# Performance work log

Measured on AMD Instinct MI355X. Metric: run time of the kernel, lower is better.

Reference implementation:

```python
import jax, jax.numpy as jnp
import numpy as np

N_NODES = 50000
N_EDGES = 800000
IN_DIM, HID_DIM, OUT_DIM = 1024, 256, 512


def setup_inputs() -> dict:
    key = jax.random.key(0)
    ks = jax.random.split(key, 8)
    x = jax.random.normal(ks[0], (N_NODES, IN_DIM), dtype=jnp.float32)
    edge_index = jax.random.randint(ks[1], (2, N_EDGES), 0, N_NODES, dtype=jnp.int64)
    # Glorot-ish scaled weights; PyG SAGEConv: out = lin_l(mean_aggr) + lin_r(x), bias in lin_l
    w1_l = jax.random.normal(ks[2], (HID_DIM, IN_DIM), dtype=jnp.float32) / np.sqrt(IN_DIM)
    w1_r = jax.random.normal(ks[3], (HID_DIM, IN_DIM), dtype=jnp.float32) / np.sqrt(IN_DIM)
    b1 = jnp.zeros((HID_DIM,), dtype=jnp.float32)
    w2_l = jax.random.normal(ks[4], (OUT_DIM, HID_DIM), dtype=jnp.float32) / np.sqrt(HID_DIM)
    w2_r = jax.random.normal(ks[5], (OUT_DIM, HID_DIM), dtype=jnp.float32) / np.sqrt(HID_DIM)
    b2 = jnp.zeros((OUT_DIM,), dtype=jnp.float32)
    return {"x": x, "edge_index": edge_index, "w1_l": w1_l, "w1_r": w1_r, "b1": b1,
            "w2_l": w2_l, "w2_r": w2_r, "b2": b2}


def _sage_conv(x, edge_index, w_l, w_r, b):
    """PyG SAGEConv with mean aggregation: lin_l(mean_{j in N(i)} x_j) + lin_r(x_i)."""
    src, dst = edge_index[0], edge_index[1]
    n = x.shape[0]
    # gather source features and scatter-mean into destinations (the memory-bound part)
    agg = jax.ops.segment_sum(x[src], dst, num_segments=n)          # [N, d_in]
    cnt = jax.ops.segment_sum(jnp.ones_like(src, dtype=x.dtype), dst, num_segments=n)
    mean = agg / jnp.maximum(cnt, 1.0)[:, None]                     # empty neighborhoods -> 0
    return mean @ w_l.T + x @ w_r.T + b


def reference(x, edge_index, w1_l, w1_r, b1, w2_l, w2_r, b2):
    # layer 1 + relu (dropout is identity in eval mode)
    h = jax.nn.relu(_sage_conv(x, edge_index, w1_l, w1_r, b1))
    # final layer, no activation
    return _sage_conv(h, edge_index, w2_l, w2_r, b2)
```

## Files before the change

### kernel.cpp

```cpp
#include <hip/hip_runtime.h>


#define IN_DIM  1024
#define HID_DIM 256
#define OUT_N   512

typedef __attribute__((ext_vector_type(8))) short bf16x8;
typedef __attribute__((ext_vector_type(4))) float f32x4;

static __device__ __forceinline__ unsigned short f2bf(float f) {
  unsigned int u = __float_as_uint(f);
  u += 0x7fffu + ((u >> 16) & 1u);
  return (unsigned short)(u >> 16);
}
static __device__ __forceinline__ float bf2f(unsigned short b) {
  return __uint_as_float(((unsigned int)b) << 16);
}

static __device__ __forceinline__ int load_idx(const void* ei, long long pos, int is64) {
  if (is64) return (int)((const long long*)ei)[pos];
  return ((const int*)ei)[pos];
}

__global__ void k_pre(const unsigned int* __restrict__ eiu, const void* __restrict__ ei,
                      int* __restrict__ flag,
                      const float* __restrict__ w1l, const float* __restrict__ w1r,
                      unsigned short* __restrict__ W1c,
                      const float* __restrict__ w2l, const float* __restrict__ w2r,
                      unsigned short* __restrict__ W2c,
                      const float* __restrict__ x, unsigned short* __restrict__ xbf,
                      int n4, int nxb, int nE, int* __restrict__ deg) {
  int b = blockIdx.x;
  if (b == 0) {
    if (threadIdx.x < 64) {
      unsigned int v = eiu[2 * threadIdx.x + 1];
      unsigned long long m = __ballot(v == 0u);
      if (threadIdx.x == 0) *flag = (m == ~0ull) ? 1 : 0;
    }
    return;
  }
  if (b < 513) {
    int i = (b - 1) * 256 + threadIdx.x;
    int base = i * 4;
    int n = base / IN_DIM, k = base % IN_DIM;
    const float* s = (n < HID_DIM) ? &w1l[(size_t)n * IN_DIM + k]
                                   : &w1r[(size_t)(n - HID_DIM) * IN_DIM + k];
    float4 v = *(const float4*)s;
    ushort4 o = { f2bf(v.x), f2bf(v.y), f2bf(v.z), f2bf(v.w) };
    *(ushort4*)&W1c[base] = o;
    return;
  }
  if (b < 769) {
    int i = (b - 513) * 256 + threadIdx.x;
    int base = i * 4;
    int n = base >> 9, k = base & 511;
    const float* s = (k < HID_DIM) ? &w2l[(size_t)n * HID_DIM + k]
                                   : &w2r[(size_t)n * HID_DIM + (k - HID_DIM)];
    float4 v = *(const float4*)s;
    ushort4 o = { f2bf(v.x), f2bf(v.y), f2bf(v.z), f2bf(v.w) };
    *(ushort4*)&W2c[base] = o;
    return;
  }
  if (b < 769 + nxb) {
    int i = (b - 769) * 256 + threadIdx.x;
    if (i >= n4) return;
    float4 v = ((const float4*)x)[i];
    ushort4 o = { f2bf(v.x), f2bf(v.y), f2bf(v.z), f2bf(v.w) };
    ((ushort4*)xbf)[i] = o;
    return;
  }
  __shared__ int s_is64;
  if (threadIdx.x < 64) {
    unsigned int v = eiu[2 * threadIdx.x + 1];
    unsigned long long m = __ballot(v == 0u);
    if (threadIdx.x == 0) s_is64 = (m == ~0ull) ? 1 : 0;
  }
  __syncthreads();
  int e = (b - 769 - nxb) * 256 + threadIdx.x;
  if (e < nE) {
    int d = load_idx(ei, (long long)nE + e, s_is64);
    atomicAdd(&deg[d], 1);
  }
}

__global__ void k_bsum(const int* __restrict__ deg, int* __restrict__ bsum) {
  int t = threadIdx.x;
  int4 d4 = ((const int4*)(deg + (size_t)blockIdx.x * 1024))[t];
  int v = d4.x + d4.y + d4.z + d4.w;
#pragma unroll
  for (int d = 1; d < 64; d <<= 1) v += __shfl_xor(v, d);
  __shared__ int ws[4];
  if ((t & 63) == 0) ws[t >> 6] = v;
  __syncthreads();
  if (t == 0) bsum[blockIdx.x] = ws[0] + ws[1] + ws[2] + ws[3];
}

__global__ __launch_bounds__(1024) void k_bscan(int* __restrict__ bsum, int nb) {
  __shared__ int s[1024];
  int t = threadIdx.x;
  s[t] = (t < nb) ? bsum[t] : 0;
  __syncthreads();
  for (int d = 1; d < 1024; d <<= 1) {
    int v = (t >= d) ? s[t - d] : 0;
    __syncthreads();
    s[t] += v;
    __syncthreads();
  }
  if (t < nb) bsum[t] = s[t];
}

__global__ __launch_bounds__(256) void k_offsets(const int* __restrict__ deg,
                                                 const int* __restrict__ bsumInc,
                                                 int* __restrict__ off,
                                                 int* __restrict__ cursor) {
  const int t = threadIdx.x;
  const int l = t & 63, w = t >> 6;
  const size_t base = (size_t)blockIdx.x * 1024;
  int4 d4 = ((const int4*)(deg + base))[t];
  int tsum = d4.x + d4.y + d4.z + d4.w;
  int incl = tsum;
#pragma unroll
  for (int d = 1; d < 64; d <<= 1) {
    int u = __shfl_up(incl, d);
    if (l >= d) incl += u;
  }
  __shared__ int wt[4];
  if (l == 63) wt[w] = incl;
  __syncthreads();
  int wpre = 0;
  for (int i = 0; i < w; ++i) wpre += wt[i];
  int bpre = (blockIdx.x == 0) ? 0 : bsumInc[blockIdx.x - 1];
  int excl = bpre + wpre + incl - tsum;
  int4 o;
  o.x = excl;
  o.y = excl + d4.x;
  o.z = o.y + d4.y;
  o.w = o.z + d4.z;
  ((int4*)(off + base))[t] = o;
  ((int4*)(cursor + base))[t] = o;
}

__global__ void k_fill(const void* ei, int nE, const int* flag,
                       int* cursor, int* __restrict__ csr) {
  int e = blockIdx.x * 256 + threadIdx.x;
  if (e >= nE) return;
  int is64 = *flag;
  int s = load_idx(ei, e, is64);
  int d = load_idx(ei, (long long)nE + e, is64);
  int p = atomicAdd(&cursor[d], 1);
  csr[p] = s;
}

static __device__ __forceinline__ void load_lds16(const void* g, void* lds) {
  __builtin_amdgcn_global_load_lds(
      (const __attribute__((address_space(1))) unsigned int*)g,
      (__attribute__((address_space(3))) unsigned int*)lds, 16, 0, 0);
}

static __device__ __forceinline__ int xcd_swz(int orig, int nwg) {
  const int q = nwg >> 3, r = nwg & 7;
  const int xcd = orig & 7, rk = orig >> 3;
  return (xcd < r) ? xcd * (q + 1) + rk : r * (q + 1) + (xcd - r) * q + rk;
}

__global__ __launch_bounds__(256) void k_gemm1(const unsigned short* __restrict__ A,
                                               const unsigned short* __restrict__ B,
                                               unsigned short* __restrict__ Cl,
                                               unsigned short* __restrict__ Cr,
                                               const float* __restrict__ b1) {
  __shared__ unsigned short As[128 * 32];
  __shared__ unsigned short Bs[128 * 32];
  const int tid = threadIdx.x;
  const int w = tid >> 6, l = tid & 63;
  const int wm = w >> 1, wn = w & 1;
  const int quad = l >> 4, lane16 = l & 15;
  const int nwg = gridDim.x * gridDim.y;
  const int wg = xcd_swz(blockIdx.y * gridDim.x + blockIdx.x, nwg);
  const int m0 = (wg / gridDim.x) * 128;
  const int n0 = (wg % gridDim.x) * 128;

  f32x4 acc[4][4] = {};
  for (int k0 = 0; k0 < IN_DIM; k0 += 32) {
#pragma unroll
    for (int c = 0; c < 2; ++c) {
      const int flat = ((w * 2 + c) << 10);
      const int fb = flat + l * 16;
      const int row = fb >> 6;
      const int cb = fb & 63;
      load_lds16(A + (size_t)(m0 + row) * IN_DIM + (k0 + (cb >> 1)), (char*)As + flat);
      load_lds16(B + (size_t)(n0 + row) * IN_DIM + (k0 + (cb >> 1)), (char*)Bs + flat);
    }
    __syncthreads();
    bf16x8 af[4], bfr[4];
#pragma unroll
    for (int i = 0; i < 4; ++i)
      af[i] = *(const bf16x8*)&As[(wm * 64 + i * 16 + lane16) * 32 + quad * 8];
#pragma unroll
    for (int j = 0; j < 4; ++j)
      bfr[j] = *(const bf16x8*)&Bs[(wn * 64 + j * 16 + lane16) * 32 + quad * 8];
#pragma unroll
    for (int i = 0; i < 4; ++i)
#pragma unroll
      for (int j = 0; j < 4; ++j)
        acc[i][j] = __builtin_amdgcn_mfma_f32_16x16x32_bf16(af[i], bfr[j], acc[i][j], 0, 0, 0);
    __syncthreads();
  }

  const bool right = (n0 >= 256);
  unsigned short* Cb = right ? Cr : Cl;
  const int nc0 = n0 - (right ? 256 : 0);
#pragma unroll
  for (int i = 0; i < 4; ++i) {
    const int rbase = m0 + wm * 64 + i * 16 + quad * 4;
#pragma unroll
    for (int j = 0; j < 4; ++j) {
      const int col = nc0 + wn * 64 + j * 16 + lane16;
      const float bv = right ? b1[col] : 0.0f;
#pragma unroll
      for (int r = 0; r < 4; ++r)
        Cb[(size_t)(rbase + r) * HID_DIM + col] = f2bf(acc[i][j][r] + bv);
    }
  }
}

__global__ __launch_bounds__(256) void k_gemm2(const unsigned short* __restrict__ Am,
                                               const unsigned short* __restrict__ Ah,
                                               const unsigned short* __restrict__ B,
                                               float* __restrict__ out,
                                               const float* __restrict__ b2, int Mstore) {
  __shared__ unsigned short As[128 * 32];
  __shared__ unsigned short Bs[128 * 32];
  const int tid = threadIdx.x;
  const int w = tid >> 6, l = tid & 63;
  const int wm = w >> 1, wn = w & 1;
  const int quad = l >> 4, lane16 = l & 15;
  const int nwg = gridDim.x * gridDim.y;
  const int wg = xcd_swz(blockIdx.y * gridDim.x + blockIdx.x, nwg);
  const int m0 = (wg / gridDim.x) * 128;
  const int n0 = (wg % gridDim.x) * 128;

  f32x4 acc[4][4] = {};
  for (int k0 = 0; k0 < 2 * HID_DIM; k0 += 32) {
    const unsigned short* Abase = (k0 < HID_DIM) ? Am + k0 : Ah + (k0 - HID_DIM);
#pragma unroll
    for (int c = 0; c < 2; ++c) {
      const int flat = ((w * 2 + c) << 10);
      const int fb = flat + l * 16;
      const int row = fb >> 6;
      const int cb = fb & 63;
      load_lds16(Abase + (size_t)(m0 + row) * HID_DIM + (cb >> 1), (char*)As + flat);
      load_lds16(B + (size_t)(n0 + row) * (2 * HID_DIM) + (k0 + (cb >> 1)), (char*)Bs + flat);
    }
    __syncthreads();
    bf16x8 af[4], bfr[4];
#pragma unroll
    for (int i = 0; i < 4; ++i)
      af[i] = *(const bf16x8*)&As[(wm * 64 + i * 16 + lane16) * 32 + quad * 8];
#pragma unroll
    for (int j = 0; j < 4; ++j)
      bfr[j] = *(const bf16x8*)&Bs[(wn * 64 + j * 16 + lane16) * 32 + quad * 8];
#pragma unroll
    for (int i = 0; i < 4; ++i)
#pragma unroll
      for (int j = 0; j < 4; ++j)
        acc[i][j] = __builtin_amdgcn_mfma_f32_16x16x32_bf16(af[i], bfr[j], acc[i][j], 0, 0, 0);
    __syncthreads();
  }

#pragma unroll
  for (int i = 0; i < 4; ++i) {
    const int rbase = m0 + wm * 64 + i * 16 + quad * 4;
#pragma unroll
    for (int j = 0; j < 4; ++j) {
      const int col = n0 + wn * 64 + j * 16 + lane16;
      const float bv = b2[col];
#pragma unroll
      for (int r = 0; r < 4; ++r) {
        const int rowi = rbase + r;
        if (rowi < Mstore) out[(size_t)rowi * OUT_N + col] = acc[i][j][r] + bv;
      }
    }
  }
}

template <int NB>
static __device__ __forceinline__ void gatherN(const unsigned short* __restrict__ src,
                                               const int* __restrict__ csr, int ib,
                                               size_t colb, float* a) {
  bf16x8 v[NB];
#pragma unroll
  for (int u = 0; u < NB; ++u) {
    int r = csr[ib + 2 * u];
    v[u] = *(const bf16x8*)&src[(size_t)r * HID_DIM + colb];
  }
#pragma unroll
  for (int u = 0; u < NB; ++u)
#pragma unroll
    for (int c = 0; c < 8; ++c) a[c] += bf2f((unsigned short)v[u][c]);
}

static __device__ __forceinline__ void agg_sum(const unsigned short* __restrict__ src,
                                               const int* __restrict__ csr,
                                               int s, int e, int half, size_t colb,
                                               float* a) {
  const int cnt = e - s;
  const int P = cnt >> 1;
  const int ib0 = s + half;
  int k = 0;
  for (; k + 8 <= P; k += 8) gatherN<8>(src, csr, ib0 + 2 * k, colb, a);
  if (k + 4 <= P) { gatherN<4>(src, csr, ib0 + 2 * k, colb, a); k += 4; }
  if (k + 2 <= P) { gatherN<2>(src, csr, ib0 + 2 * k, colb, a); k += 2; }
  if (k < P)      { gatherN<1>(src, csr, ib0 + 2 * k, colb, a); }
  if ((cnt & 1) && half == 0) {
    bf16x8 v = *(const bf16x8*)&src[(size_t)csr[e - 1] * HID_DIM + colb];
#pragma unroll
    for (int c = 0; c < 8; ++c) a[c] += bf2f((unsigned short)v[c]);
  }
#pragma unroll
  for (int c = 0; c < 8; ++c) a[c] += __shfl_xor(a[c], 32);
}

__global__ void k_agg1(const unsigned short* __restrict__ Cl,
                       const unsigned short* __restrict__ Cr,
                       const int* __restrict__ off, const int* __restrict__ csr,
                       unsigned short* __restrict__ h, int nNodes) {
  int node = blockIdx.x * 4 + (threadIdx.x >> 6);
  if (node >= nNodes) return;
  const int l = threadIdx.x & 63;
  const int half = l >> 5, li = l & 31;
  const size_t colb = (size_t)li * 8;
  int s = off[node], e = off[node + 1];
  float a[8] = {};
  agg_sum(Cl, csr, s, e, half, colb, a);
  if (half == 0) {
    float inv = 1.0f / fmaxf((float)(e - s), 1.0f);
    bf16x8 xr = *(const bf16x8*)&Cr[(size_t)node * HID_DIM + colb];
    bf16x8 o;
#pragma unroll
    for (int c = 0; c < 8; ++c)
      o[c] = (short)f2bf(fmaxf(a[c] * inv + bf2f((unsigned short)xr[c]), 0.0f));
    *(bf16x8*)&h[(size_t)node * HID_DIM + colb] = o;
  }
}

__global__ void k_agg2(const unsigned short* __restrict__ hsrc,
                       const int* __restrict__ off, const int* __restrict__ csr,
                       unsigned short* __restrict__ mean2, int nNodes) {
  int node = blockIdx.x * 4 + (threadIdx.x >> 6);
  if (node >= nNodes) return;
  const int l = threadIdx.x & 63;
  const int half = l >> 5, li = l & 31;
  const size_t colb = (size_t)li * 8;
  int s = off[node], e = off[node + 1];
  float a[8] = {};
  agg_sum(hsrc, csr, s, e, half, colb, a);
  if (half == 0) {
    float inv = 1.0f / fmaxf((float)(e - s), 1.0f);
    bf16x8 o;
#pragma unroll
    for (int c = 0; c < 8; ++c) o[c] = (short)f2bf(a[c] * inv);
    *(bf16x8*)&mean2[(size_t)node * HID_DIM + colb] = o;
  }
}

extern "C" void kernel_launch(void* const* d_in, const int* in_sizes, int n_in,
                              void* d_out, int out_size, void* d_ws, size_t ws_size,
                              hipStream_t stream) {
  const float* x   = (const float*)d_in[0];
  const void*  ei  = d_in[1];
  const float* w1l = (const float*)d_in[2];
  const float* w1r = (const float*)d_in[3];
  const float* b1  = (const float*)d_in[4];
  const float* w2l = (const float*)d_in[5];
  const float* w2r = (const float*)d_in[6];
  const float* b2  = (const float*)d_in[7];
  float* out = (float*)d_out;

  const int nN   = in_sizes[0] / IN_DIM;
  const int nE   = in_sizes[1] / 2;
  const int Mpad = (nN + 127) & ~127;
  const int padN = (nN + 1023) & ~1023;
  const int nb   = padN >> 10;

  char* ws = (char*)d_ws;
  size_t o = 0;
  auto alloc = [&](size_t bytes) {
    char* p = ws + o;
    o += (bytes + 255) & ~(size_t)255;
    return p;
  };
  unsigned short* xbf   = (unsigned short*)alloc((size_t)Mpad * IN_DIM * 2);
  unsigned short* W1c   = (unsigned short*)alloc((size_t)2 * HID_DIM * IN_DIM * 2);
  unsigned short* W2c   = (unsigned short*)alloc((size_t)OUT_N * 2 * HID_DIM * 2);
  unsigned short* Cl    = (unsigned short*)alloc((size_t)Mpad * HID_DIM * 2);
  unsigned short* Cr    = (unsigned short*)alloc((size_t)Mpad * HID_DIM * 2);
  unsigned short* hbuf  = (unsigned short*)alloc((size_t)Mpad * HID_DIM * 2);
  unsigned short* mean2 = (unsigned short*)alloc((size_t)Mpad * HID_DIM * 2);
  int* deg    = (int*)alloc((size_t)padN * 4);
  int* offs   = (int*)alloc((size_t)padN * 4);
  int* cursor = (int*)alloc((size_t)padN * 4);
  int* bsum   = (int*)alloc((size_t)1024 * 4);
  int* csr    = (int*)alloc((size_t)nE * 4);
  int* flag   = (int*)alloc(256);

  hipMemsetAsync(deg, 0, (size_t)padN * 4, stream);

  const int n4  = nN * IN_DIM / 4;
  const int nxb = (n4 + 255) / 256;
  const int nEb = (nE + 255) / 256;
  k_pre<<<769 + nxb + nEb, 256, 0, stream>>>((const unsigned int*)ei, ei, flag,
                                             w1l, w1r, W1c, w2l, w2r, W2c,
                                             x, xbf, n4, nxb, nE, deg);
  k_bsum<<<nb, 256, 0, stream>>>(deg, bsum);
  k_bscan<<<1, 1024, 0, stream>>>(bsum, nb);
  k_offsets<<<nb, 256, 0, stream>>>(deg, bsum, offs, cursor);
  k_fill<<<(nE + 255) / 256, 256, 0, stream>>>(ei, nE, flag, cursor, csr);

  dim3 g1(512 / 128, Mpad / 128);
  k_gemm1<<<g1, 256, 0, stream>>>(xbf, W1c, Cl, Cr, b1);
  k_agg1<<<(nN + 3) / 4, 256, 0, stream>>>(Cl, Cr, offs, csr, hbuf, nN);
  k_agg2<<<(nN + 3) / 4, 256, 0, stream>>>(hbuf, offs, csr, mean2, nN);
  k_gemm2<<<g1, 256, 0, stream>>>(mean2, hbuf, W2c, out, b2, nN);
}
```

Measured before the change: 667.7 us.

## Fuse x bf16 conversion into GEMM1, merge scan kernels, overlap CSR fill

Drops the separate pass that converted x to bf16. GEMM1 now loads fp32 x directly, converts it in registers and stores it to LDS, which saves a full write and re-read of a 100MB-class intermediate. The three-kernel degree prefix scan becomes a single one-block scan kernel. The CSR fill runs as extra blocks appended to the GEMM1 grid so it overlaps the GEMM. In exchange, the A loads in the GEMM lose async direct-to-LDS transfer and become synchronous, and the single-block scan serializes roughly 50K entries.

Result: no change. 654.9 us (-1.9%).

```diff
diff --git a/kernel.cpp b/kernel.cpp
--- a/kernel.cpp
+++ b/kernel.cpp
@@ -28,8 +28,7 @@
                       unsigned short* __restrict__ W1c,
                       const float* __restrict__ w2l, const float* __restrict__ w2r,
                       unsigned short* __restrict__ W2c,
-                      const float* __restrict__ x, unsigned short* __restrict__ xbf,
-                      int n4, int nxb, int nE, int* __restrict__ deg) {
+                      int nE, int* __restrict__ deg) {
   int b = blockIdx.x;
   if (b == 0) {
     if (threadIdx.x < 64) {
@@ -61,14 +60,6 @@
     *(ushort4*)&W2c[base] = o;
     return;
   }
-  if (b < 769 + nxb) {
-    int i = (b - 769) * 256 + threadIdx.x;
-    if (i >= n4) return;
-    float4 v = ((const float4*)x)[i];
-    ushort4 o = { f2bf(v.x), f2bf(v.y), f2bf(v.z), f2bf(v.w) };
-    ((ushort4*)xbf)[i] = o;
-    return;
-  }
   __shared__ int s_is64;
   if (threadIdx.x < 64) {
     unsigned int v = eiu[2 * threadIdx.x + 1];
@@ -76,79 +67,51 @@
     if (threadIdx.x == 0) s_is64 = (m == ~0ull) ? 1 : 0;
   }
   __syncthreads();
-  int e = (b - 769 - nxb) * 256 + threadIdx.x;
+  int e = (b - 769) * 256 + threadIdx.x;
   if (e < nE) {
     int d = load_idx(ei, (long long)nE + e, s_is64);
     atomicAdd(&deg[d], 1);
   }
 }
 
-__global__ void k_bsum(const int* __restrict__ deg, int* __restrict__ bsum) {
-  int t = threadIdx.x;
-  int4 d4 = ((const int4*)(deg + (size_t)blockIdx.x * 1024))[t];
-  int v = d4.x + d4.y + d4.z + d4.w;
-#pragma unroll
-  for (int d = 1; d < 64; d <<= 1) v += __shfl_xor(v, d);
-  __shared__ int ws[4];
-  if ((t & 63) == 0) ws[t >> 6] = v;
-  __syncthreads();
-  if (t == 0) bsum[blockIdx.x] = ws[0] + ws[1] + ws[2] + ws[3];
-}
-
-__global__ __launch_bounds__(1024) void k_bscan(int* __restrict__ bsum, int nb) {
+__global__ __launch_bounds__(1024) void k_scan1(const int* __restrict__ deg,
+                                                int* __restrict__ off,
+                                                int* __restrict__ cursor, int n4q) {
+  const int t = threadIdx.x;
+  const int CH = (n4q + 1023) >> 10;
+  const int i0 = t * CH;
+  int tsum = 0;
+  for (int i = 0; i < CH; ++i) {
+    int idx = i0 + i;
+    if (idx < n4q) {
+      int4 d = ((const int4*)deg)[idx];
+      tsum += d.x + d.y + d.z + d.w;
+    }
+  }
   __shared__ int s[1024];
-  int t = threadIdx.x;
-  s[t] = (t < nb) ? bsum[t] : 0;
+  s[t] = tsum;
   __syncthreads();
   for (int d = 1; d < 1024; d <<= 1) {
-    int v = (t >= d) ? s[t - d] : 0;
-    __syncthreads();
-    s[t] += v;
-    __syncthreads();
-  }
-  if (t < nb) bsum[t] = s[t];
-}
-
-__global__ __launch_bounds__(256) void k_offsets(const int* __restrict__ deg,
-                                                 const int* __restrict__ bsumInc,
-                                                 int* __restrict__ off,
-                                                 int* __restrict__ cursor) {
-  const int t = threadIdx.x;
-  const int l = t & 63, w = t >> 6;
-  const size_t base = (size_t)blockIdx.x * 1024;
-  int4 d4 = ((const int4*)(deg + base))[t];
-  int tsum = d4.x + d4.y + d4.z + d4.w;
-  int incl = tsum;
-#pragma unroll
-  for (int d = 1; d < 64; d <<= 1) {
-    int u = __shfl_up(incl, d);
-    if (l >= d) incl += u;
-  }
-  __shared__ int wt[4];
-  if (l == 63) wt[w] = incl;
-  __syncthreads();
-  int wpre = 0;
-  for (int i = 0; i < w; ++i) wpre += wt[i];
-  int bpre = (blockIdx.x == 0) ? 0 : bsumInc[blockIdx.x - 1];
-  int excl = bpre + wpre + incl - tsum;
-  int4 o;
-  o.x = excl;
-  o.y = excl + d4.x;
-  o.z = o.y + d4.y;
-  o.w = o.z + d4.z;
-  ((int4*)(off + base))[t] = o;
-  ((int4*)(cursor + base))[t] = o;
-}
-
-__global__ void k_fill(const void* ei, int nE, const int* flag,
-                       int* cursor, int* __restrict__ csr) {
-  int e = blockIdx.x * 256 + threadIdx.x;
-  if (e >= nE) return;
-  int is64 = *flag;
-  int s = load_idx(ei, e, is64);
-  int d = load_idx(ei, (long long)nE + e, is64);
-  int p = atomicAdd(&cursor[d], 1);
-  csr[p] = s;
+    int u = (t >= d) ? s[t - d] : 0;
+    __syncthreads();
+    s[t] += u;
+    __syncthreads();
+  }
+  int run = (t == 0) ? 0 : s[t - 1];
+  for (int i = 0; i < CH; ++i) {
+    int idx = i0 + i;
+    if (idx < n4q) {
+      int4 d = ((const int4*)deg)[idx];
+      int4 o;
+      o.x = run;
+      o.y = run + d.x;
+      o.z = o.y + d.y;
+      o.w = o.z + d.z;
+      run = o.w + d.w;
+      ((int4*)off)[idx] = o;
+      ((int4*)cursor)[idx] = o;
+    }
+  }
 }
 
 static __device__ __forceinline__ void load_lds16(const void* g, void* lds) {
@@ -163,31 +126,61 @@
   return (xcd < r) ? xcd * (q + 1) + rk : r * (q + 1) + (xcd - r) * q + rk;
 }
 
-__global__ __launch_bounds__(256) void k_gemm1(const unsigned short* __restrict__ A,
-                                               const unsigned short* __restrict__ B,
-                                               unsigned short* __restrict__ Cl,
-                                               unsigned short* __restrict__ Cr,
-                                               const float* __restrict__ b1) {
+__global__ __launch_bounds__(256) void k_g1f(const float* __restrict__ A,
+                                             const unsigned short* __restrict__ B,
+                                             unsigned short* __restrict__ Cl,
+                                             unsigned short* __restrict__ Cr,
+                                             const float* __restrict__ b1,
+                                             int nNm1, int ngemm,
+                                             const void* __restrict__ ei, int nE,
+                                             const int* __restrict__ flag,
+                                             int* __restrict__ cursor,
+                                             int* __restrict__ csr) {
+  if ((int)blockIdx.x >= ngemm) {
+    int e = ((int)blockIdx.x - ngemm) * 256 + threadIdx.x;
+    if (e < nE) {
+      int is64 = *flag;
+      int s = load_idx(ei, e, is64);
+      int d = load_idx(ei, (long long)nE + e, is64);
+      int p = atomicAdd(&cursor[d], 1);
+      csr[p] = s;
+    }
+    return;
+  }
   __shared__ unsigned short As[128 * 32];
   __shared__ unsigned short Bs[128 * 32];
   const int tid = threadIdx.x;
   const int w = tid >> 6, l = tid & 63;
   const int wm = w >> 1, wn = w & 1;
   const int quad = l >> 4, lane16 = l & 15;
-  const int nwg = gridDim.x * gridDim.y;
-  const int wg = xcd_swz(blockIdx.y * gridDim.x + blockIdx.x, nwg);
-  const int m0 = (wg / gridDim.x) * 128;
-  const int n0 = (wg % gridDim.x) * 128;
+  const int wg = xcd_swz(blockIdx.x, ngemm);
+  const int m0 = (wg >> 2) * 128;
+  const int n0 = (wg & 3) * 128;
+
+  const float* ap[4];
+#pragma unroll
+  for (int it = 0; it < 4; ++it) {
+    const int eidx = it * 1024 + tid * 4;
+    int ar = m0 + (eidx >> 5);
+    if (ar > nNm1) ar = nNm1;
+    ap[it] = A + (size_t)ar * IN_DIM + (eidx & 31);
+  }
 
   f32x4 acc[4][4] = {};
   for (int k0 = 0; k0 < IN_DIM; k0 += 32) {
+#pragma unroll
+    for (int it = 0; it < 4; ++it) {
+      const int eidx = it * 1024 + tid * 4;
+      float4 v = *(const float4*)(ap[it] + k0);
+      ushort4 o = { f2bf(v.x), f2bf(v.y), f2bf(v.z), f2bf(v.w) };
+      *(ushort4*)&As[eidx] = o;
+    }
 #pragma unroll
     for (int c = 0; c < 2; ++c) {
       const int flat = ((w * 2 + c) << 10);
       const int fb = flat + l * 16;
       const int row = fb >> 6;
       const int cb = fb & 63;
-      load_lds16(A + (size_t)(m0 + row) * IN_DIM + (k0 + (cb >> 1)), (char*)As + flat);
       load_lds16(B + (size_t)(n0 + row) * IN_DIM + (k0 + (cb >> 1)), (char*)Bs + flat);
     }
     __syncthreads();
@@ -380,7 +373,6 @@
   const int nE   = in_sizes[1] / 2;
   const int Mpad = (nN + 127) & ~127;
   const int padN = (nN + 1023) & ~1023;
-  const int nb   = padN >> 10;
 
   char* ws = (char*)d_ws;
   size_t o = 0;
@@ -389,7 +381,6 @@
     o += (bytes + 255) & ~(size_t)255;
     return p;
   };
-  unsigned short* xbf   = (unsigned short*)alloc((size_t)Mpad * IN_DIM * 2);
   unsigned short* W1c   = (unsigned short*)alloc((size_t)2 * HID_DIM * IN_DIM * 2);
   unsigned short* W2c   = (unsigned short*)alloc((size_t)OUT_N * 2 * HID_DIM * 2);
   unsigned short* Cl    = (unsigned short*)alloc((size_t)Mpad * HID_DIM * 2);
@@ -399,26 +390,21 @@
   int* deg    = (int*)alloc((size_t)padN * 4);
   int* offs   = (int*)alloc((size_t)padN * 4);
   int* cursor = (int*)alloc((size_t)padN * 4);
-  int* bsum   = (int*)alloc((size_t)1024 * 4);
   int* csr    = (int*)alloc((size_t)nE * 4);
   int* flag   = (int*)alloc(256);
 
   hipMemsetAsync(deg, 0, (size_t)padN * 4, stream);
 
-  const int n4  = nN * IN_DIM / 4;
-  const int nxb = (n4 + 255) / 256;
-  const int nEb = (nE + 255) / 256;
-  k_pre<<<769 + nxb + nEb, 256, 0, stream>>>((const unsigned int*)ei, ei, flag,
-                                             w1l, w1r, W1c, w2l, w2r, W2c,
-                                             x, xbf, n4, nxb, nE, deg);
-  k_bsum<<<nb, 256, 0, stream>>>(deg, bsum);
-  k_bscan<<<1, 1024, 0, stream>>>(bsum, nb);
-  k_offsets<<<nb, 256, 0, stream>>>(deg, bsum, offs, cursor);
-  k_fill<<<(nE + 255) / 256, 256, 0, stream>>>(ei, nE, flag, cursor, csr);
-
-  dim3 g1(512 / 128, Mpad / 128);
-  k_gemm1<<<g1, 256, 0, stream>>>(xbf, W1c, Cl, Cr, b1);
+  const int nEb   = (nE + 255) / 256;
+  const int ngemm = 4 * (Mpad / 128);
+
+  k_pre<<<769 + nEb, 256, 0, stream>>>((const unsigned int*)ei, ei, flag,
+                                       w1l, w1r, W1c, w2l, w2r, W2c, nE, deg);
+  k_scan1<<<1, 1024, 0, stream>>>(deg, offs, cursor, padN / 4);
+  k_g1f<<<ngemm + nEb, 256, 0, stream>>>(x, W1c, Cl, Cr, b1, nN - 1, ngemm,
+                                         ei, nE, flag, cursor, csr);
   k_agg1<<<(nN + 3) / 4, 256, 0, stream>>>(Cl, Cr, offs, csr, hbuf, nN);
   k_agg2<<<(nN + 3) / 4, 256, 0, stream>>>(hbuf, offs, csr, mean2, nN);
-  k_gemm2<<<g1, 256, 0, stream>>>(mean2, hbuf, W2c, out, b2, nN);
-}
+  dim3 g2(512 / 128, Mpad / 128);
+  k_gemm2<<<g2, 256, 0, stream>>>(mean2, hbuf, W2c, out, b2, nN);
+}
```

## Double-buffer GEMM LDS tiles and fuse CSR fill into GEMM1 launch

Applied to the files above, without the earlier changes.

Both GEMM kernels now use two LDS buffers, so the tile for the next K step is loaded while MFMAs run on the current one, with one barrier per iteration instead of two. The CSR fill kernel is merged into the first GEMM launch as extra blocks, so the atomic edge scatter runs alongside the GEMM instead of as a separate launch. This doubles LDS per block, which may lower occupancy, and the fill blocks compete with GEMM blocks for CUs.

Result: no change. 675.2 us (+1.1%).

```diff
diff --git a/kernel.cpp b/kernel.cpp
--- a/kernel.cpp
+++ b/kernel.cpp
@@ -140,17 +140,6 @@
   ((int4*)(cursor + base))[t] = o;
 }
 
-__global__ void k_fill(const void* ei, int nE, const int* flag,
-                       int* cursor, int* __restrict__ csr) {
-  int e = blockIdx.x * 256 + threadIdx.x;
-  if (e >= nE) return;
-  int is64 = *flag;
-  int s = load_idx(ei, e, is64);
-  int d = load_idx(ei, (long long)nE + e, is64);
-  int p = atomicAdd(&cursor[d], 1);
-  csr[p] = s;
-}
-
 static __device__ __forceinline__ void load_lds16(const void* g, void* lds) {
   __builtin_amdgcn_global_load_lds(
       (const __attribute__((address_space(1))) unsigned int*)g,
@@ -163,13 +152,98 @@
   return (xcd < r) ? xcd * (q + 1) + rk : r * (q + 1) + (xcd - r) * q + rk;
 }
 
-__global__ __launch_bounds__(256) void k_gemm1(const unsigned short* __restrict__ A,
+__global__ __launch_bounds__(256) void k_g1f(const unsigned short* __restrict__ A,
+                                             const unsigned short* __restrict__ B,
+                                             unsigned short* __restrict__ Cl,
+                                             unsigned short* __restrict__ Cr,
+                                             const float* __restrict__ b1,
+                                             int ngemm,
+                                             const void* __restrict__ ei, int nE,
+                                             const int* __restrict__ flag,
+                                             int* __restrict__ cursor,
+                                             int* __restrict__ csr) {
+  if ((int)blockIdx.x >= ngemm) {
+    int e = ((int)blockIdx.x - ngemm) * 256 + threadIdx.x;
+    if (e < nE) {
+      int is64 = *flag;
+      int s = load_idx(ei, e, is64);
+      int d = load_idx(ei, (long long)nE + e, is64);
+      int p = atomicAdd(&cursor[d], 1);
+      csr[p] = s;
+    }
+    return;
+  }
+  __shared__ unsigned short As[2][128 * 32];
+  __shared__ unsigned short Bs[2][128 * 32];
+  const int tid = threadIdx.x;
+  const int w = tid >> 6, l = tid & 63;
+  const int wm = w >> 1, wn = w & 1;
+  const int quad = l >> 4, lane16 = l & 15;
+  const int wg = xcd_swz(blockIdx.x, ngemm);
+  const int m0 = (wg >> 2) * 128;
+  const int n0 = (wg & 3) * 128;
+
+  const int flat0 = ((w * 2 + 0) << 10), flat1 = ((w * 2 + 1) << 10);
+  const int row0 = (flat0 + l * 16) >> 6, cb0 = (flat0 + l * 16) & 63;
+  const int row1 = (flat1 + l * 16) >> 6, cb1 = (flat1 + l * 16) & 63;
+  const unsigned short* Ar0 = A + (size_t)(m0 + row0) * IN_DIM + (cb0 >> 1);
+  const unsigned short* Ar1 = A + (size_t)(m0 + row1) * IN_DIM + (cb1 >> 1);
+  const unsigned short* Br0 = B + (size_t)(n0 + row0) * IN_DIM + (cb0 >> 1);
+  const unsigned short* Br1 = B + (size_t)(n0 + row1) * IN_DIM + (cb1 >> 1);
+
+  auto STAGE = [&](int k0, int buf) {
+    load_lds16(Ar0 + k0, (char*)As[buf] + flat0);
+    load_lds16(Br0 + k0, (char*)Bs[buf] + flat0);
+    load_lds16(Ar1 + k0, (char*)As[buf] + flat1);
+    load_lds16(Br1 + k0, (char*)Bs[buf] + flat1);
+  };
+
+  f32x4 acc[4][4] = {};
+  STAGE(0, 0);
+  __syncthreads();
+  int cur = 0;
+  for (int k0 = 0; k0 < IN_DIM; k0 += 32) {
+    if (k0 + 32 < IN_DIM) STAGE(k0 + 32, cur ^ 1);
+    bf16x8 af[4], bfr[4];
+#pragma unroll
+    for (int i = 0; i < 4; ++i)
+      af[i] = *(const bf16x8*)&As[cur][(wm * 64 + i * 16 + lane16) * 32 + quad * 8];
+#pragma unroll
+    for (int j = 0; j < 4; ++j)
+      bfr[j] = *(const bf16x8*)&Bs[cur][(wn * 64 + j * 16 + lane16) * 32 + quad * 8];
+#pragma unroll
+    for (int i = 0; i < 4; ++i)
+#pragma unroll
+      for (int j = 0; j < 4; ++j)
+        acc[i][j] = __builtin_amdgcn_mfma_f32_16x16x32_bf16(af[i], bfr[j], acc[i][j], 0, 0, 0);
+    __syncthreads();
+    cur ^= 1;
+  }
+
+  const bool right = (n0 >= 256);
+  unsigned short* Cb = right ? Cr : Cl;
+  const int nc0 = n0 - (right ? 256 : 0);
+#pragma unroll
+  for (int i = 0; i < 4; ++i) {
+    const int rbase = m0 + wm * 64 + i * 16 + quad * 4;
+#pragma unroll
+    for (int j = 0; j < 4; ++j) {
+      const int col = nc0 + wn * 64 + j * 16 + lane16;
+      const float bv = right ? b1[col] : 0.0f;
+#pragma unroll
+      for (int r = 0; r < 4; ++r)
+        Cb[(size_t)(rbase + r) * HID_DIM + col] = f2bf(acc[i][j][r] + bv);
+    }
+  }
+}
+
+__global__ __launch_bounds__(256) void k_gemm2(const unsigned short* __restrict__ Am,
+                                               const unsigned short* __restrict__ Ah,
                                                const unsigned short* __restrict__ B,
-                                               unsigned short* __restrict__ Cl,
-                                               unsigned short* __restrict__ Cr,
-                                               const float* __restrict__ b1) {
-  __shared__ unsigned short As[128 * 32];
-  __shared__ unsigned short Bs[128 * 32];
+                                               float* __restrict__ out,
+                                               const float* __restrict__ b2, int Mstore) {
+  __shared__ unsigned short As[2][128 * 32];
+  __shared__ unsigned short Bs[2][128 * 32];
   const int tid = threadIdx.x;
   const int w = tid >> 6, l = tid & 63;
   const int wm = w >> 1, wn = w & 1;
@@ -179,92 +253,38 @@
   const int m0 = (wg / gridDim.x) * 128;
   const int n0 = (wg % gridDim.x) * 128;
 
+  const int flat0 = ((w * 2 + 0) << 10), flat1 = ((w * 2 + 1) << 10);
+  const int row0 = (flat0 + l * 16) >> 6, cb0 = (flat0 + l * 16) & 63;
+  const int row1 = (flat1 + l * 16) >> 6, cb1 = (flat1 + l * 16) & 63;
+
+  auto STAGE = [&](int kk, int buf) {
+    const unsigned short* Abase = (kk < HID_DIM) ? Am + kk : Ah + (kk - HID_DIM);
+    load_lds16(Abase + (size_t)(m0 + row0) * HID_DIM + (cb0 >> 1), (char*)As[buf] + flat0);
+    load_lds16(B + (size_t)(n0 + row0) * (2 * HID_DIM) + (kk + (cb0 >> 1)), (char*)Bs[buf] + flat0);
+    load_lds16(Abase + (size_t)(m0 + row1) * HID_DIM + (cb1 >> 1), (char*)As[buf] + flat1);
+    load_lds16(B + (size_t)(n0 + row1) * (2 * HID_DIM) + (kk + (cb1 >> 1)), (char*)Bs[buf] + flat1);
+  };
+
   f32x4 acc[4][4] = {};
-  for (int k0 = 0; k0 < IN_DIM; k0 += 32) {
-#pragma unroll
-    for (int c = 0; c < 2; ++c) {
-      const int flat = ((w * 2 + c) << 10);
-      const int fb = flat + l * 16;
-      const int row = fb >> 6;
-      const int cb = fb & 63;
-      load_lds16(A + (size_t)(m0 + row) * IN_DIM + (k0 + (cb >> 1)), (char*)As + flat);
-      load_lds16(B + (size_t)(n0 + row) * IN_DIM + (k0 + (cb >> 1)), (char*)Bs + flat);
-    }
-    __syncthreads();
+  STAGE(0, 0);
+  __syncthreads();
+  int cur = 0;
+  for (int k0 = 0; k0 < 2 * HID_DIM; k0 += 32) {
+    if (k0 + 32 < 2 * HID_DIM) STAGE(k0 + 32, cur ^ 1);
     bf16x8 af[4], bfr[4];
 #pragma unroll
     for (int i = 0; i < 4; ++i)
-      af[i] = *(const bf16x8*)&As[(wm * 64 + i * 16 + lane16) * 32 + quad * 8];
+      af[i] = *(const bf16x8*)&As[cur][(wm * 64 + i * 16 + lane16) * 32 + quad * 8];
 #pragma unroll
     for (int j = 0; j < 4; ++j)
-      bfr[j] = *(const bf16x8*)&Bs[(wn * 64 + j * 16 + lane16) * 32 + quad * 8];
+      bfr[j] = *(const bf16x8*)&Bs[cur][(wn * 64 + j * 16 + lane16) * 32 + quad * 8];
 #pragma unroll
     for (int i = 0; i < 4; ++i)
 #pragma unroll
       for (int j = 0; j < 4; ++j)
         acc[i][j] = __builtin_amdgcn_mfma_f32_16x16x32_bf16(af[i], bfr[j], acc[i][j], 0, 0, 0);
     __syncthreads();
-  }
-
-  const bool right = (n0 >= 256);
-  unsigned short* Cb = right ? Cr : Cl;
-  const int nc0 = n0 - (right ? 256 : 0);
-#pragma unroll
-  for (int i = 0; i < 4; ++i) {
-    const int rbase = m0 + wm * 64 + i * 16 + quad * 4;
-#pragma unroll
-    for (int j = 0; j < 4; ++j) {
-      const int col = nc0 + wn * 64 + j * 16 + lane16;
-      const float bv = right ? b1[col] : 0.0f;
-#pragma unroll
-      for (int r = 0; r < 4; ++r)
-        Cb[(size_t)(rbase + r) * HID_DIM + col] = f2bf(acc[i][j][r] + bv);
-    }
-  }
-}
-
-__global__ __launch_bounds__(256) void k_gemm2(const unsigned short* __restrict__ Am,
-                                               const unsigned short* __restrict__ Ah,
-                                               const unsigned short* __restrict__ B,
-                                               float* __restrict__ out,
-                                               const float* __restrict__ b2, int Mstore) {
-  __shared__ unsigned short As[128 * 32];
-  __shared__ unsigned short Bs[128 * 32];
-  const int tid = threadIdx.x;
-  const int w = tid >> 6, l = tid & 63;
-  const int wm = w >> 1, wn = w & 1;
-  const int quad = l >> 4, lane16 = l & 15;
-  const int nwg = gridDim.x * gridDim.y;
-  const int wg = xcd_swz(blockIdx.y * gridDim.x + blockIdx.x, nwg);
-  const int m0 = (wg / gridDim.x) * 128;
-  const int n0 = (wg % gridDim.x) * 128;
-
-  f32x4 acc[4][4] = {};
-  for (int k0 = 0; k0 < 2 * HID_DIM; k0 += 32) {
-    const unsigned short* Abase = (k0 < HID_DIM) ? Am + k0 : Ah + (k0 - HID_DIM);
-#pragma unroll
-    for (int c = 0; c < 2; ++c) {
-      const int flat = ((w * 2 + c) << 10);
-      const int fb = flat + l * 16;
-      const int row = fb >> 6;
-      const int cb = fb & 63;
-      load_lds16(Abase + (size_t)(m0 + row) * HID_DIM + (cb >> 1), (char*)As + flat);
-      load_lds16(B + (size_t)(n0 + row) * (2 * HID_DIM) + (k0 + (cb >> 1)), (char*)Bs + flat);
-    }
-    __syncthreads();
-    bf16x8 af[4], bfr[4];
-#pragma unroll
-    for (int i = 0; i < 4; ++i)
-      af[i] = *(const bf16x8*)&As[(wm * 64 + i * 16 + lane16) * 32 + quad * 8];
-#pragma unroll
-    for (int j = 0; j < 4; ++j)
-      bfr[j] = *(const bf16x8*)&Bs[(wn * 64 + j * 16 + lane16) * 32 + quad * 8];
-#pragma unroll
-    for (int i = 0; i < 4; ++i)
-#pragma unroll
-      for (int j = 0; j < 4; ++j)
-        acc[i][j] = __builtin_amdgcn_mfma_f32_16x16x32_bf16(af[i], bfr[j], acc[i][j], 0, 0, 0);
-    __syncthreads();
+    cur ^= 1;
   }
 
 #pragma unroll
@@ -408,17 +428,18 @@
   const int n4  = nN * IN_DIM / 4;
   const int nxb = (n4 + 255) / 256;
   const int nEb = (nE + 255) / 256;
+  const int ngemm = 4 * (Mpad / 128);
+
   k_pre<<<769 + nxb + nEb, 256, 0, stream>>>((const unsigned int*)ei, ei, flag,
                                              w1l, w1r, W1c, w2l, w2r, W2c,
                                              x, xbf, n4, nxb, nE, deg);
   k_bsum<<<nb, 256, 0, stream>>>(deg, bsum);
   k_bscan<<<1, 1024, 0, stream>>>(bsum, nb);
   k_offsets<<<nb, 256, 0, stream>>>(deg, bsum, offs, cursor);
-  k_fill<<<(nE + 255) / 256, 256, 0, stream>>>(ei, nE, flag, cursor, csr);
-
-  dim3 g1(512 / 128, Mpad / 128);
-  k_gemm1<<<g1, 256, 0, stream>>>(xbf, W1c, Cl, Cr, b1);
+  k_g1f<<<ngemm + nEb, 256, 0, stream>>>(xbf, W1c, Cl, Cr, b1, ngemm,
+                                         ei, nE, flag, cursor, csr);
   k_agg1<<<(nN + 3) / 4, 256, 0, stream>>>(Cl, Cr, offs, csr, hbuf, nN);
   k_agg2<<<(nN + 3) / 4, 256, 0, stream>>>(hbuf, offs, csr, mean2, nN);
-  k_gemm2<<<g1, 256, 0, stream>>>(mean2, hbuf, W2c, out, b2, nN);
-}
+  dim3 g2(512 / 128, Mpad / 128);
+  k_gemm2<<<g2, 256, 0, stream>>>(mean2, hbuf, W2c, out, b2, nN);
+}
```
